# Performance work log

Hardware: AMD Instinct MI355X
Metric: run time of the kernel (lower is better)

## Reference

```python
import jax, jax.numpy as jnp
import numpy as np

D_MODEL = 768
D_INNER = 1536   # expand=2
D_STATE = 16
D_CONV = 4
DT_RANK = 48     # ceil(768/16)
B_SZ, L = 2, 2048


def _mamba(h, in_proj, conv_w, conv_b, xproj, dtproj_w, dtproj_b, A_log, Dskip, out_proj):
    """One Mamba block forward. h: [B, L, d_model]."""
    B = h.shape[0]
    xz = h @ in_proj.T                      # [B, L, 2*d_inner]
    x, z = jnp.split(xz, 2, axis=-1)
    # causal depthwise conv over time
    xc = jnp.transpose(x, (0, 2, 1))        # [B, D, L]
    xc = jax.lax.conv_general_dilated(
        xc, conv_w[:, None, :], (1,), [(D_CONV - 1, 0)],
        dimension_numbers=('NCH', 'OIH', 'NCH'), feature_group_count=D_INNER)
    xc = xc + conv_b[None, :, None]
    x = jax.nn.silu(jnp.transpose(xc, (0, 2, 1)))   # [B, L, D]
    # input-dependent dt, B, C
    dbl = x @ xproj.T                                # [B, L, dt_rank + 2*d_state]
    dt, Bm, Cm = jnp.split(dbl, [DT_RANK, DT_RANK + D_STATE], axis=-1)
    dt = jax.nn.softplus(dt @ dtproj_w.T + dtproj_b) # [B, L, D]
    A = -jnp.exp(A_log)                              # [D, N]

    def step(hst, inp):
        x_t, dt_t, B_t, C_t = inp                    # [B,D],[B,D],[B,N],[B,N]
        dA = jnp.exp(dt_t[..., None] * A)            # [B, D, N]
        hst = hst * dA + dt_t[..., None] * B_t[:, None, :] * x_t[..., None]
        y = jnp.einsum('bdn,bn->bd', hst, C_t)
        return hst, y

    h0 = jnp.zeros((B, D_INNER, D_STATE), dtype=h.dtype)
    xs = (jnp.transpose(x, (1, 0, 2)), jnp.transpose(dt, (1, 0, 2)),
          jnp.transpose(Bm, (1, 0, 2)), jnp.transpose(Cm, (1, 0, 2)))
    _, ys = jax.lax.scan(step, h0, xs)               # ys: [L, B, D]
    y = jnp.transpose(ys, (1, 0, 2)) + x * Dskip
    y = y * jax.nn.silu(z)
    return y @ out_proj.T                            # [B, L, d_model]


def _init_params(key):
    ks = jax.random.split(key, 7)
    s = 0.02
    in_proj = jax.random.normal(ks[0], (2 * D_INNER, D_MODEL)) * s
    conv_w = jax.random.normal(ks[1], (D_INNER, D_CONV)) * 0.2
    conv_b = jnp.zeros((D_INNER,))
    xproj = jax.random.normal(ks[2], (DT_RANK + 2 * D_STATE, D_INNER)) * s
    dtproj_w = jax.random.normal(ks[3], (D_INNER, DT_RANK)) * (DT_RANK ** -0.5)
    dtproj_b = jnp.log(jax.random.uniform(ks[4], (D_INNER,), minval=1e-3, maxval=0.1))
    A_log = jnp.log(jnp.tile(jnp.arange(1, D_STATE + 1, dtype=jnp.float32), (D_INNER, 1)))
    Dskip = jnp.ones((D_INNER,))
    out_proj = jax.random.normal(ks[5], (D_MODEL, D_INNER)) * s
    return in_proj, conv_w, conv_b, xproj, dtproj_w, dtproj_b, A_log, Dskip, out_proj


def setup_inputs() -> dict:
    key = jax.random.key(0)
    k_h, k_f, k_r = jax.random.split(key, 3)
    inp = {'hidden_states': jax.random.normal(k_h, (B_SZ, L, D_MODEL), dtype=jnp.float32)}
    names = ['in_proj', 'conv_w', 'conv_b', 'xproj', 'dtproj_w', 'dtproj_b', 'A_log', 'Dskip', 'out_proj']
    for suf, k in (('_f', k_f), ('_r', k_r)):
        for n, p in zip(names, _init_params(k)):
            inp[n + suf] = p
    return inp


def reference(hidden_states,
              in_proj_f, conv_w_f, conv_b_f, xproj_f, dtproj_w_f, dtproj_b_f, A_log_f, Dskip_f, out_proj_f,
              in_proj_r, conv_w_r, conv_b_r, xproj_r, dtproj_w_r, dtproj_b_r, A_log_r, Dskip_r, out_proj_r):
    out = _mamba(hidden_states, in_proj_f, conv_w_f, conv_b_f, xproj_f,
                 dtproj_w_f, dtproj_b_f, A_log_f, Dskip_f, out_proj_f)
    out_rev = _mamba(hidden_states[:, ::-1, :], in_proj_r, conv_w_r, conv_b_r, xproj_r,
                     dtproj_w_r, dtproj_b_r, A_log_r, Dskip_r, out_proj_r)[:, ::-1, :]
    return out + out_rev
```

## Files before the change

### kernel.cpp

```cpp
#include <hip/hip_runtime.h>
#include <hip/hip_bf16.h>
#include <math.h>

#define L_SEQ 2048
#define B_SZ 2
#define D_MODEL 768
#define D_INNER 1536
#define D_STATE 16
#define DT_RANK 48
#define TC 64
#define NC (L_SEQ / TC)
#define NDG (D_INNER / 256)
#define NSPL 4
#define KCH (D_INNER / NSPL)

typedef short bf16x8 __attribute__((ext_vector_type(8)));
typedef float f32x4 __attribute__((ext_vector_type(4)));

#define GLOAD16(g, l) __builtin_amdgcn_global_load_lds( \
    (const __attribute__((address_space(1))) unsigned*)(g), \
    (__attribute__((address_space(3))) unsigned*)(l), 16, 0, 0)

static __device__ __forceinline__ float siluf(float v) {
  return v / (1.0f + __expf(-v));
}
static __device__ __forceinline__ float softplusf(float v) {
  return fmaxf(v, 0.0f) + log1pf(__expf(-fabsf(v)));
}
static __device__ __forceinline__ unsigned short f2bf_rn(float v) {
  unsigned u = __float_as_uint(v);
  u = (u + 0x7fff + ((u >> 16) & 1)) >> 16;
  return (unsigned short)u;
}

__global__ __launch_bounds__(256) void cvt_all(
    const float* __restrict__ s_h,  unsigned short* __restrict__ hh,  unsigned short* __restrict__ hl,
    const float* __restrict__ s_w0, unsigned short* __restrict__ w0h, unsigned short* __restrict__ w0l,
    const float* __restrict__ s_w1, unsigned short* __restrict__ w1h, unsigned short* __restrict__ w1l,
    const float* __restrict__ s_o0, unsigned short* __restrict__ o0h, unsigned short* __restrict__ o0l,
    const float* __restrict__ s_o1, unsigned short* __restrict__ o1h, unsigned short* __restrict__ o1l)
{
  long j = (long)blockIdx.x * 256 + threadIdx.x;
  const long N0 = 786432, N1 = 589824, N2 = 589824, N3 = 294912;
  const float* src; unsigned short *dh, *dl;
  if (j < N0) { src = s_h; dh = hh; dl = hl; }
  else if ((j -= N0) < N1) { src = s_w0; dh = w0h; dl = w0l; }
  else if ((j -= N1) < N2) { src = s_w1; dh = w1h; dl = w1l; }
  else if ((j -= N2) < N3) { src = s_o0; dh = o0h; dl = o0l; }
  else { j -= N3; src = s_o1; dh = o1h; dl = o1l; }
  float4 v = ((const float4*)src)[j];
  float vv[4] = {v.x, v.y, v.z, v.w};
  unsigned short h4[4], l4[4];
  #pragma unroll
  for (int e = 0; e < 4; ++e) {
    unsigned short hv = f2bf_rn(vv[e]);
    h4[e] = hv;
    l4[e] = f2bf_rn(vv[e] - __uint_as_float((unsigned)hv << 16));
  }
  uint2 ph, pl;
  ph.x = (unsigned)h4[0] | ((unsigned)h4[1] << 16);
  ph.y = (unsigned)h4[2] | ((unsigned)h4[3] << 16);
  pl.x = (unsigned)l4[0] | ((unsigned)l4[1] << 16);
  pl.y = (unsigned)l4[2] | ((unsigned)l4[3] << 16);
  *(uint2*)&dh[j * 4] = ph;
  *(uint2*)&dl[j * 4] = pl;
}

__global__ __launch_bounds__(256) void gemm_inproj(
    const unsigned short* __restrict__ hh, const unsigned short* __restrict__ hl,
    const unsigned short* __restrict__ w0h, const unsigned short* __restrict__ w0l,
    const unsigned short* __restrict__ w1h, const unsigned short* __restrict__ w1l,
    float* __restrict__ xpre, float* __restrict__ zbuf)
{
  __shared__ unsigned short Ah[128 * 32], Al[128 * 32];
  __shared__ unsigned short Wh[128 * 32], Wl[128 * 32];
  const long S1 = (long)B_SZ * L_SEQ * D_INNER;
  const int tid = threadIdx.x;
  const int lane = tid & 63, w = tid >> 6;
  int bid = blockIdx.x;
  int swz = (bid & 7) * 192 + (bid >> 3);
  int dir = swz / 768;
  int rem = swz - dir * 768;
  int mb = rem / 24, nb = rem - (rem / 24) * 24;
  const int m0 = mb * 128, n0 = nb * 128;
  const unsigned short* Whp = dir ? w1h : w0h;
  const unsigned short* Wlp = dir ? w1l : w0l;
  const int ksl = (lane & 3) ^ ((lane >> 3) & 3);
  long aoff[2], woff[2];
  int ldsc[2];
  #pragma unroll
  for (int qq = 0; qq < 2; ++qq) {
    int cq = w * 2 + qq;
    int r = cq * 16 + (lane >> 2);
    int mr = m0 + r;
    int row = dir ? ((mr & ~(L_SEQ - 1)) | ((L_SEQ - 1) - (mr & (L_SEQ - 1)))) : mr;
    aoff[qq] = (long)row * D_MODEL + 8 * ksl;
    woff[qq] = (long)(n0 + r) * D_MODEL + 8 * ksl;
    ldsc[qq] = cq * 512;
  }
  f32x4 acc[4][4];
  #pragma unroll
  for (int i = 0; i < 4; ++i)
    #pragma unroll
    for (int j = 0; j < 4; ++j) acc[i][j] = (f32x4){0.f, 0.f, 0.f, 0.f};
  const int fr = lane & 15, sl = lane >> 4;
  const int wr = w >> 1, wc = w & 1;
  int roffA[4], roffW[4];
  #pragma unroll
  for (int f = 0; f < 4; ++f) {
    int rA = wr * 64 + f * 16 + fr;
    roffA[f] = rA * 32 + ((sl ^ ((rA >> 1) & 3)) * 8);
    int rW = wc * 64 + f * 16 + fr;
    roffW[f] = rW * 32 + ((sl ^ ((rW >> 1) & 3)) * 8);
  }
  for (int k0 = 0; k0 < D_MODEL; k0 += 32) {
    __syncthreads();
    #pragma unroll
    for (int qq = 0; qq < 2; ++qq) {
      GLOAD16(hh + aoff[qq] + k0, &Ah[ldsc[qq]]);
      GLOAD16(hl + aoff[qq] + k0, &Al[ldsc[qq]]);
      GLOAD16(Whp + woff[qq] + k0, &Wh[ldsc[qq]]);
      GLOAD16(Wlp + woff[qq] + k0, &Wl[ldsc[qq]]);
    }
    __syncthreads();
    bf16x8 afh[4], afl[4];
    #pragma unroll
    for (int f = 0; f < 4; ++f) {
      afh[f] = *(const bf16x8*)&Ah[roffA[f]];
      afl[f] = *(const bf16x8*)&Al[roffA[f]];
    }
    #pragma unroll
    for (int fj = 0; fj < 4; ++fj) {
      bf16x8 wfh = *(const bf16x8*)&Wh[roffW[fj]];
      bf16x8 wfl = *(const bf16x8*)&Wl[roffW[fj]];
      #pragma unroll
      for (int fi = 0; fi < 4; ++fi) {
        acc[fi][fj] = __builtin_amdgcn_mfma_f32_16x16x32_bf16(afh[fi], wfh, acc[fi][fj], 0, 0, 0);
        acc[fi][fj] = __builtin_amdgcn_mfma_f32_16x16x32_bf16(afh[fi], wfl, acc[fi][fj], 0, 0, 0);
        acc[fi][fj] = __builtin_amdgcn_mfma_f32_16x16x32_bf16(afl[fi], wfh, acc[fi][fj], 0, 0, 0);
      }
    }
  }
  float* xq = xpre + (long)dir * S1;
  float* zq = zbuf + (long)dir * S1;
  const int fcol = lane & 15, rgrp = lane >> 4;
  #pragma unroll
  for (int fi = 0; fi < 4; ++fi) {
    #pragma unroll
    for (int j = 0; j < 4; ++j) {
      int row = m0 + wr * 64 + fi * 16 + rgrp * 4 + j;
      #pragma unroll
      for (int fj = 0; fj < 4; ++fj) {
        int n = n0 + wc * 64 + fj * 16 + fcol;
        float v = acc[fi][fj][j];
        if (n < D_INNER) xq[(long)row * D_INNER + n] = v;
        else             zq[(long)row * D_INNER + (n - D_INNER)] = v;
      }
    }
  }
}

__global__ __launch_bounds__(256) void gemm_outproj_sk(
    const float* __restrict__ y,
    const unsigned short* __restrict__ wfh, const unsigned short* __restrict__ wfl,
    const unsigned short* __restrict__ wrh, const unsigned short* __restrict__ wrl,
    float* __restrict__ partial)
{
  __shared__ unsigned short Ah[128 * 32], Al[128 * 32];
  __shared__ unsigned short Wh[128 * 32], Wl[128 * 32];
  const long S1 = (long)B_SZ * L_SEQ * D_INNER;
  const int tid = threadIdx.x;
  const int lane = tid & 63, w = tid >> 6;
  int bid = blockIdx.x;
  int swz = (bid & 7) * 96 + (bid >> 3);
  int dir = swz / 384;
  int r1 = swz - dir * 384;
  int ks = r1 / 192;
  int r2 = r1 - ks * 192;
  int mb = r2 / 6, nb = r2 - (r2 / 6) * 6;
  const int m0 = mb * 128, n0 = nb * 128;
  const int kbase = ks * (D_INNER / 2);
  const int srow = tid >> 1, sk = (tid & 1) * 16;
  const int swzA = (srow >> 1) & 3;
  {
  }
  int mr = m0 + srow;
  int rowA = dir ? ((mr & ~(L_SEQ - 1)) | ((L_SEQ - 1) - (mr & (L_SEQ - 1)))) : mr;
  const float* Aptr = y + (long)dir * S1 + (long)rowA * D_INNER + sk;
  const unsigned short* WhP = dir ? wrh : wfh;
  const unsigned short* WlP = dir ? wrl : wfl;
  const int ksl = (lane & 3) ^ ((lane >> 3) & 3);
  long woff[2];
  int ldsc[2];
  #pragma unroll
  for (int qq = 0; qq < 2; ++qq) {
    int cq = w * 2 + qq;
    int r = cq * 16 + (lane >> 2);
    woff[qq] = (long)(n0 + r) * D_INNER + 8 * ksl;
    ldsc[qq] = cq * 512;
  }
  f32x4 acc[4][4];
  #pragma unroll
  for (int i = 0; i < 4; ++i)
    #pragma unroll
    for (int j = 0; j < 4; ++j) acc[i][j] = (f32x4){0.f, 0.f, 0.f, 0.f};
  const int fr = lane & 15, sl = lane >> 4;
  const int wr = w >> 1, wc = w & 1;
  int roffA[4], roffW[4];
  #pragma unroll
  for (int f = 0; f < 4; ++f) {
    int rA = wr * 64 + f * 16 + fr;
    roffA[f] = rA * 32 + ((sl ^ ((rA >> 1) & 3)) * 8);
    int rW = wc * 64 + f * 16 + fr;
    roffW[f] = rW * 32 + ((sl ^ ((rW >> 1) & 3)) * 8);
  }
  for (int k0 = kbase; k0 < kbase + D_INNER / 2; k0 += 32) {
    float4 av[4];
    #pragma unroll
    for (int q = 0; q < 4; ++q) av[q] = *(const float4*)(Aptr + k0 + q * 4);
    unsigned short ah[16], al[16];
    #pragma unroll
    for (int q = 0; q < 4; ++q) {
      float va[4] = {av[q].x, av[q].y, av[q].z, av[q].w};
      #pragma unroll
      for (int e = 0; e < 4; ++e) {
        int i = q * 4 + e;
        unsigned short hv = f2bf_rn(va[e]);
        ah[i] = hv;
        al[i] = f2bf_rn(va[e] - __uint_as_float((unsigned)hv << 16));
      }
    }
    __syncthreads();
    #pragma unroll
    for (int qq = 0; qq < 2; ++qq) {
      GLOAD16(WhP + woff[qq] + k0, &Wh[ldsc[qq]]);
      GLOAD16(WlP + woff[qq] + k0, &Wl[ldsc[qq]]);
    }
    #pragma unroll
    for (int s = 0; s < 2; ++s) {
      int slot = (sk >> 3) + s;
      int off = srow * 32 + ((slot ^ swzA) * 8);
      *(bf16x8*)&Ah[off] = *(const bf16x8*)&ah[s * 8];
      *(bf16x8*)&Al[off] = *(const bf16x8*)&al[s * 8];
    }
    __syncthreads();
    bf16x8 afh[4], afl[4];
    #pragma unroll
    for (int f = 0; f < 4; ++f) {
      afh[f] = *(const bf16x8*)&Ah[roffA[f]];
      afl[f] = *(const bf16x8*)&Al[roffA[f]];
    }
    #pragma unroll
    for (int fj = 0; fj < 4; ++fj) {
      bf16x8 wh = *(const bf16x8*)&Wh[roffW[fj]];
      bf16x8 wl = *(const bf16x8*)&Wl[roffW[fj]];
      #pragma unroll
      for (int fi = 0; fi < 4; ++fi) {
        acc[fi][fj] = __builtin_amdgcn_mfma_f32_16x16x32_bf16(afh[fi], wh, acc[fi][fj], 0, 0, 0);
        acc[fi][fj] = __builtin_amdgcn_mfma_f32_16x16x32_bf16(afh[fi], wl, acc[fi][fj], 0, 0, 0);
        acc[fi][fj] = __builtin_amdgcn_mfma_f32_16x16x32_bf16(afl[fi], wh, acc[fi][fj], 0, 0, 0);
      }
    }
  }
  float* P = partial + (long)(dir * 2 + ks) * (B_SZ * L_SEQ) * D_MODEL;
  const int fcol = lane & 15, rgrp = lane >> 4;
  #pragma unroll
  for (int fi = 0; fi < 4; ++fi) {
    #pragma unroll
    for (int j = 0; j < 4; ++j) {
      int row = m0 + wr * 64 + fi * 16 + rgrp * 4 + j;
      #pragma unroll
      for (int fj = 0; fj < 4; ++fj) {
        int n = n0 + wc * 64 + fj * 16 + fcol;
        P[(long)row * D_MODEL + n] = acc[fi][fj][j];
      }
    }
  }
}

__global__ __launch_bounds__(256) void outproj_reduce(
    const float* __restrict__ partial, float* __restrict__ out)
{
  long i = (long)blockIdx.x * 256 + threadIdx.x;
  const long plane4 = (long)B_SZ * L_SEQ * D_MODEL / 4;
  float4 a = ((const float4*)partial)[i];
  float4 b = ((const float4*)partial)[i + plane4];
  float4 c = ((const float4*)partial)[i + 2 * plane4];
  float4 d = ((const float4*)partial)[i + 3 * plane4];
  float4 s;
  s.x = (a.x + b.x) + (c.x + d.x);
  s.y = (a.y + b.y) + (c.y + d.y);
  s.z = (a.z + b.z) + (c.z + d.z);
  s.w = (a.w + b.w) + (c.w + d.w);
  ((float4*)out)[i] = s;
}

__global__ __launch_bounds__(256) void dtproj(
    const float* __restrict__ dblB,
    const float* __restrict__ w_f, const float* __restrict__ w_r,
    const float* __restrict__ b_f, const float* __restrict__ b_r,
    float* __restrict__ dtOut)
{
  const int dir = blockIdx.z;
  const float* A = dblB + (long)dir * (B_SZ * L_SEQ) * 80;
  const float* W = dir ? w_r : w_f;
  const float* bias = dir ? b_r : b_f;
  float* C0 = dtOut + (long)dir * B_SZ * L_SEQ * D_INNER;
  __shared__ float As[16][132];
  __shared__ float Ws[16][132];
  const int tid = threadIdx.x;
  const int m0 = blockIdx.y * 128, n0 = blockIdx.x * 128;
  const int tx = tid & 15, ty = tid >> 4;
  const int lm = tid >> 1;
  const int lk = (tid & 1) * 8;
  const float* Aptr = A + (long)(m0 + lm) * 80 + lk;
  const float* Wptr = W + (long)(n0 + lm) * DT_RANK + lk;
  float acc[8][8] = {};
  for (int k0 = 0; k0 < DT_RANK; k0 += 16) {
    float4 a0 = *(const float4*)(Aptr + k0);
    float4 a1 = *(const float4*)(Aptr + k0 + 4);
    float4 w0 = *(const float4*)(Wptr + k0);
    float4 w1 = *(const float4*)(Wptr + k0 + 4);
    As[lk + 0][lm] = a0.x; As[lk + 1][lm] = a0.y; As[lk + 2][lm] = a0.z; As[lk + 3][lm] = a0.w;
    As[lk + 4][lm] = a1.x; As[lk + 5][lm] = a1.y; As[lk + 6][lm] = a1.z; As[lk + 7][lm] = a1.w;
    Ws[lk + 0][lm] = w0.x; Ws[lk + 1][lm] = w0.y; Ws[lk + 2][lm] = w0.z; Ws[lk + 3][lm] = w0.w;
    Ws[lk + 4][lm] = w1.x; Ws[lk + 5][lm] = w1.y; Ws[lk + 6][lm] = w1.z; Ws[lk + 7][lm] = w1.w;
    __syncthreads();
    #pragma unroll
    for (int kk = 0; kk < 16; ++kk) {
      float4 av0 = *(const float4*)&As[kk][ty * 4];
      float4 av1 = *(const float4*)&As[kk][64 + ty * 4];
      float4 bv0 = *(const float4*)&Ws[kk][tx * 4];
      float4 bv1 = *(const float4*)&Ws[kk][64 + tx * 4];
      float am[8] = {av0.x, av0.y, av0.z, av0.w, av1.x, av1.y, av1.z, av1.w};
      float bn[8] = {bv0.x, bv0.y, bv0.z, bv0.w, bv1.x, bv1.y, bv1.z, bv1.w};
      #pragma unroll
      for (int i = 0; i < 8; ++i)
        #pragma unroll
        for (int j = 0; j < 8; ++j) acc[i][j] = fmaf(am[i], bn[j], acc[i][j]);
    }
    __syncthreads();
  }
  #pragma unroll
  for (int i = 0; i < 8; ++i) {
    int row = m0 + ty * 4 + (i & 3) + ((i >> 2) << 6);
    #pragma unroll
    for (int j = 0; j < 8; ++j) {
      int n = n0 + tx * 4 + (j & 3) + ((j >> 2) << 6);
      float v = acc[i][j] + bias[n];
      C0[(long)row * D_INNER + n] = softplusf(v);
    }
  }
}

__global__ __launch_bounds__(256) void xproj_splitk(
    const float* __restrict__ X,
    const float* __restrict__ xproj_f, const float* __restrict__ xproj_r,
    float* __restrict__ partial)
{
  const int tid = threadIdx.x;
  const int m0 = blockIdx.x * 64;
  const int kz = blockIdx.y;
  const int dir = blockIdx.z;
  const float* W = dir ? xproj_r : xproj_f;
  const float* A = X + (long)dir * B_SZ * L_SEQ * D_INNER;
  __shared__ float As[16][65];
  __shared__ float Ws[16][81];
  const int lk = tid & 15, lr = tid >> 4;
  const int tx = tid & 15, ty = tid >> 4;
  float acc[4][5] = {};
  const int kbase = kz * KCH;
  for (int k0 = 0; k0 < KCH; k0 += 16) {
    #pragma unroll
    for (int i = 0; i < 4; ++i)
      As[lk][lr + 16 * i] = A[(long)(m0 + lr + 16 * i) * D_INNER + kbase + k0 + lk];
    for (int r = lr; r < 80; r += 16)
      Ws[lk][r] = W[(long)r * D_INNER + kbase + k0 + lk];
    __syncthreads();
    #pragma unroll
    for (int kk = 0; kk < 16; ++kk) {
      float a[4], b[5];
      #pragma unroll
      for (int i = 0; i < 4; ++i) a[i] = As[kk][ty + 16 * i];
      #pragma unroll
      for (int j = 0; j < 5; ++j) b[j] = Ws[kk][tx * 5 + j];
      #pragma unroll
      for (int i = 0; i < 4; ++i)
        #pragma unroll
        for (int j = 0; j < 5; ++j) acc[i][j] = fmaf(a[i], b[j], acc[i][j]);
    }
    __syncthreads();
  }
  float* P = partial + (((long)dir * NSPL + kz) * (B_SZ * L_SEQ) + m0) * 80;
  #pragma unroll
  for (int i = 0; i < 4; ++i)
    #pragma unroll
    for (int j = 0; j < 5; ++j)
      P[(long)(ty + 16 * i) * 80 + tx * 5 + j] = acc[i][j];
}

__global__ __launch_bounds__(256) void xproj_reduce(
    const float* __restrict__ partial, float* __restrict__ dbl)
{
  long idx = (long)blockIdx.x * 256 + threadIdx.x;
  const long plane = (long)B_SZ * L_SEQ * 80;
  long dir = idx / plane;
  long rc = idx % plane;
  const float* P = partial + dir * NSPL * plane + rc;
  float s = 0.f;
  #pragma unroll
  for (int z = 0; z < NSPL; ++z) s += P[z * plane];
  dbl[idx] = s;
}

__global__ __launch_bounds__(256) void conv_silu_v4(
    const float* __restrict__ xpre,
    const float* __restrict__ w_f, const float* __restrict__ b_f,
    const float* __restrict__ w_r, const float* __restrict__ b_r,
    float* __restrict__ xconv)
{
  long i4 = (long)blockIdx.x * 256 + threadIdx.x;
  const long total4 = 2L * B_SZ * L_SEQ * D_INNER / 4;
  if (i4 >= total4) return;
  long idx = i4 * 4;
  int d0 = (int)(idx % D_INNER);
  long r = idx / D_INNER;
  int t = (int)(r & (L_SEQ - 1));
  int dir = (int)(r >> 12);
  const float* w  = dir ? w_r : w_f;
  const float* cb = dir ? b_r : b_f;
  float4 a = *(const float4*)&cb[d0];
  float4 wc[4];
  #pragma unroll
  for (int i = 0; i < 4; ++i) wc[i] = *(const float4*)&w[(d0 + i) * 4];
  #pragma unroll
  for (int k = 0; k < 4; ++k) {
    if (t - 3 + k >= 0) {
      float4 xv = *(const float4*)&xpre[(r - 3 + k) * D_INNER + d0];
      a.x = fmaf(((const float*)&wc[0])[k], xv.x, a.x);
      a.y = fmaf(((const float*)&wc[1])[k], xv.y, a.y);
      a.z = fmaf(((const float*)&wc[2])[k], xv.z, a.z);
      a.w = fmaf(((const float*)&wc[3])[k], xv.w, a.w);
    }
  }
  a.x = siluf(a.x); a.y = siluf(a.y); a.z = siluf(a.z); a.w = siluf(a.w);
  *(float4*)&xconv[idx] = a;
}

__global__ __launch_bounds__(256) void scan_part1(
    const float* __restrict__ dt, const float* __restrict__ x,
    const float* __restrict__ dbl,
    const float* __restrict__ A_log_f, const float* __restrict__ A_log_r,
    float* __restrict__ stateS, float* __restrict__ stateP)
{
  const int tid = threadIdx.x;
  const int chunk = blockIdx.x / NDG;
  const int d = (blockIdx.x % NDG) * 256 + tid;
  const int b = blockIdx.y, dir = blockIdx.z;
  const float* A_log = dir ? A_log_r : A_log_f;
  float Arow[D_STATE];
  #pragma unroll
  for (int n = 0; n < D_STATE; ++n) Arow[n] = -expf(A_log[d * D_STATE + n]);
  float h[D_STATE], P[D_STATE];
  #pragma unroll
  for (int n = 0; n < D_STATE; ++n) { h[n] = 0.f; P[n] = 1.f; }
  const long rowbase = ((long)dir * B_SZ + b) * L_SEQ + (long)chunk * TC;
  __shared__ float bt[TC][D_STATE];
  for (int i = tid; i < TC * D_STATE; i += 256) {
    int t = i >> 4, n = i & 15;
    bt[t][n] = dbl[(rowbase + t) * 80 + 48 + n];
  }
  __syncthreads();
  for (int tj = 0; tj < TC; ++tj) {
    long off = (rowbase + tj) * D_INNER + d;
    float dtv = dt[off];
    float xv = x[off];
    float dtx = dtv * xv;
    #pragma unroll
    for (int n = 0; n < D_STATE; ++n) {
      float dA = __expf(dtv * Arow[n]);
      P[n] *= dA;
      h[n] = fmaf(h[n], dA, dtx * bt[tj][n]);
    }
  }
  long base = ((((long)dir * B_SZ + b) * NC + chunk) * D_INNER + d) * D_STATE;
  #pragma unroll
  for (int n = 0; n < D_STATE; ++n) { stateS[base + n] = h[n]; stateP[base + n] = P[n]; }
}

__global__ __launch_bounds__(256) void scan_fix(
    float* __restrict__ stateS, const float* __restrict__ stateP)
{
  const long idx = (long)blockIdx.x * 256 + threadIdx.x;
  const int DN = D_INNER * D_STATE;
  const long dirb = idx / DN;
  const int dn = (int)(idx % DN);
  long base = dirb * NC * DN + dn;
  float h = 0.f;
  for (int c = 0; c < NC; ++c) {
    long o = base + (long)c * DN;
    float S = stateS[o];
    float Pc = stateP[o];
    stateS[o] = h;
    h = fmaf(h, Pc, S);
  }
}

__global__ __launch_bounds__(256) void scan_part2(
    const float* __restrict__ dt, float* __restrict__ xy,
    const float* __restrict__ dbl, const float* __restrict__ z,
    const float* __restrict__ A_log_f, const float* __restrict__ A_log_r,
    const float* __restrict__ Ds_f, const float* __restrict__ Ds_r,
    const float* __restrict__ stateS)
{
  const int tid = threadIdx.x;
  const int chunk = blockIdx.x / NDG;
  const int d = (blockIdx.x % NDG) * 256 + tid;
  const int b = blockIdx.y, dir = blockIdx.z;
  const float* A_log = dir ? A_log_r : A_log_f;
  const float* Ds = dir ? Ds_r : Ds_f;
  float Arow[D_STATE];
  #pragma unroll
  for (int n = 0; n < D_STATE; ++n) Arow[n] = -expf(A_log[d * D_STATE + n]);
  const float Dd = Ds[d];
  float h[D_STATE];
  long sbase = ((((long)dir * B_SZ + b) * NC + chunk) * D_INNER + d) * D_STATE;
  #pragma unroll
  for (int n = 0; n < D_STATE; ++n) h[n] = stateS[sbase + n];
  const long rowbase = ((long)dir * B_SZ + b) * L_SEQ + (long)chunk * TC;
  __shared__ float bc[TC][2 * D_STATE];
  for (int i = tid; i < TC * 2 * D_STATE; i += 256) {
    int t = i >> 5, n = i & 31;
    bc[t][n] = dbl[(rowbase + t) * 80 + 48 + n];
  }
  __syncthreads();
  for (int tj = 0; tj < TC; ++tj) {
    long off = (rowbase + tj) * D_INNER + d;
    float dtv = dt[off];
    float xv = xy[off];
    float zv = z[off];
    float dtx = dtv * xv;
    float y = 0.f;
    #pragma unroll
    for (int n = 0; n < D_STATE; ++n) {
      float dA = __expf(dtv * Arow[n]);
      h[n] = fmaf(h[n], dA, dtx * bc[tj][n]);
      y = fmaf(h[n], bc[tj][16 + n], y);
    }
    y = fmaf(xv, Dd, y);
    y *= siluf(zv);
    xy[off] = y;
  }
}

extern "C" void kernel_launch(void* const* d_in, const int* in_sizes, int n_in,
                              void* d_out, int out_size, void* d_ws, size_t ws_size,
                              hipStream_t stream) {
  const float* h        = (const float*)d_in[0];
  const float* in_proj[2] = {(const float*)d_in[1], (const float*)d_in[10]};
  const float* conv_w[2]  = {(const float*)d_in[2], (const float*)d_in[11]};
  const float* conv_b[2]  = {(const float*)d_in[3], (const float*)d_in[12]};
  const float* xproj[2]   = {(const float*)d_in[4], (const float*)d_in[13]};
  const float* dtw[2]     = {(const float*)d_in[5], (const float*)d_in[14]};
  const float* dtb[2]     = {(const float*)d_in[6], (const float*)d_in[15]};
  const float* A_log[2]   = {(const float*)d_in[7], (const float*)d_in[16]};
  const float* Dsk[2]     = {(const float*)d_in[8], (const float*)d_in[17]};
  const float* outp[2]    = {(const float*)d_in[9], (const float*)d_in[18]};
  float* out = (float*)d_out;
  float* ws = (float*)d_ws;

  const long S1 = (long)B_SZ * L_SEQ * D_INNER;
  const int M = B_SZ * L_SEQ;
  float* xpre  = ws;
  float* zbuf  = ws + 2 * S1;
  float* xconv = ws + 4 * S1;
  float* dbl   = ws + 6 * S1;
  float* base4 = dbl + 2L * M * 80;

  unsigned short* hh  = (unsigned short*)base4;
  unsigned short* hl  = hh + 3145728;
  unsigned short* w0h = hl + 3145728;
  unsigned short* w0l = w0h + 2359296;
  unsigned short* w1h = w0l + 2359296;
  unsigned short* w1l = w1h + 2359296;
  unsigned short* o0h = w1l + 2359296;
  unsigned short* o0l = o0h + 1179648;
  unsigned short* o1h = o0l + 1179648;
  unsigned short* o1l = o1h + 1179648;
  float* xpartial = base4;
  float* stS = base4;
  float* stP = stS + 3145728;
  float* opartial = xpre;

  dim3 blk(256);

  cvt_all<<<dim3(9984), blk, 0, stream>>>(
      h, hh, hl, in_proj[0], w0h, w0l, in_proj[1], w1h, w1l,
      outp[0], o0h, o0l, outp[1], o1h, o1l);

  gemm_inproj<<<dim3(1536), blk, 0, stream>>>(hh, hl, w0h, w0l, w1h, w1l, xpre, zbuf);

  conv_silu_v4<<<dim3((unsigned)(2 * S1 / 4 / 256)), blk, 0, stream>>>(
      xpre, conv_w[0], conv_b[0], conv_w[1], conv_b[1], xconv);

  {
    dim3 grid(M / 64, NSPL, 2);
    xproj_splitk<<<grid, blk, 0, stream>>>(xconv, xproj[0], xproj[1], xpartial);
    long n = 2L * M * 80;
    xproj_reduce<<<dim3((unsigned)(n / 256)), blk, 0, stream>>>(xpartial, dbl);
  }
  {
    dim3 grid(D_INNER / 128, M / 128, 2);
    dtproj<<<grid, blk, 0, stream>>>(dbl, dtw[0], dtw[1], dtb[0], dtb[1], xpre);
  }
  {
    dim3 grid1(NC * NDG, B_SZ, 2);
    scan_part1<<<grid1, blk, 0, stream>>>(xpre, xconv, dbl,
        A_log[0], A_log[1], stS, stP);
    long nfix = 2L * B_SZ * D_INNER * D_STATE;
    scan_fix<<<dim3((unsigned)(nfix / 256)), blk, 0, stream>>>(stS, stP);
    scan_part2<<<grid1, blk, 0, stream>>>(xpre, xconv, dbl, zbuf,
        A_log[0], A_log[1], Dsk[0], Dsk[1], stS);
  }
  gemm_outproj_sk<<<dim3(768), blk, 0, stream>>>(xconv, o0h, o0l, o1h, o1l, opartial);
  outproj_reduce<<<dim3((unsigned)(M * (long)D_MODEL / 4 / 256)), blk, 0, stream>>>(opartial, out);
}
```

Baseline: 508.7 us.

## Fuse dt projection into scan kernels and emit split-bf16 y for out_proj

Removes the separate dtproj GEMM. Each scan thread now keeps its 48 dt-projection weights in registers and recomputes dt plus softplus per timestep from the dbl row, in both scan passes. The second scan pass writes y already split into bf16 hi/lo halves, so the out-projection GEMM can load A tiles straight into LDS with global_load_lds instead of converting fp32 in the loop. This saves the dt tensor's write and read traffic and one launch, but doubles the dt compute (it runs in both passes) and raises register pressure in the scan kernels.

```diff
diff --git a/kernel.cpp b/kernel.cpp
--- a/kernel.cpp
+++ b/kernel.cpp
@@ -160,10 +160,10 @@
   }
 }
 
-__global__ __launch_bounds__(256) void gemm_outproj_sk(
-    const float* __restrict__ y,
-    const unsigned short* __restrict__ wfh, const unsigned short* __restrict__ wfl,
-    const unsigned short* __restrict__ wrh, const unsigned short* __restrict__ wrl,
+__global__ __launch_bounds__(256) void gemm_outproj_pl(
+    const unsigned short* __restrict__ yh, const unsigned short* __restrict__ yl,
+    const unsigned short* __restrict__ o0h, const unsigned short* __restrict__ o0l,
+    const unsigned short* __restrict__ o1h, const unsigned short* __restrict__ o1l,
     float* __restrict__ partial)
 {
   __shared__ unsigned short Ah[128 * 32], Al[128 * 32];
@@ -180,23 +180,21 @@
   int mb = r2 / 6, nb = r2 - (r2 / 6) * 6;
   const int m0 = mb * 128, n0 = nb * 128;
   const int kbase = ks * (D_INNER / 2);
-  const int srow = tid >> 1, sk = (tid & 1) * 16;
-  const int swzA = (srow >> 1) & 3;
-  {
-  }
-  int mr = m0 + srow;
-  int rowA = dir ? ((mr & ~(L_SEQ - 1)) | ((L_SEQ - 1) - (mr & (L_SEQ - 1)))) : mr;
-  const float* Aptr = y + (long)dir * S1 + (long)rowA * D_INNER + sk;
-  const unsigned short* WhP = dir ? wrh : wfh;
-  const unsigned short* WlP = dir ? wrl : wfl;
+  const unsigned short* Ahp = yh + (long)dir * S1;
+  const unsigned short* Alp = yl + (long)dir * S1;
+  const unsigned short* Whp = dir ? o1h : o0h;
+  const unsigned short* Wlp = dir ? o1l : o0l;
   const int ksl = (lane & 3) ^ ((lane >> 3) & 3);
-  long woff[2];
+  long aoff[2], woff[2];
   int ldsc[2];
   #pragma unroll
   for (int qq = 0; qq < 2; ++qq) {
     int cq = w * 2 + qq;
     int r = cq * 16 + (lane >> 2);
-    woff[qq] = (long)(n0 + r) * D_INNER + 8 * ksl;
+    int mr = m0 + r;
+    int row = dir ? ((mr & ~(L_SEQ - 1)) | ((L_SEQ - 1) - (mr & (L_SEQ - 1)))) : mr;
+    aoff[qq] = (long)row * D_INNER + 8 * ksl + kbase;
+    woff[qq] = (long)(n0 + r) * D_INNER + 8 * ksl + kbase;
     ldsc[qq] = cq * 512;
   }
   f32x4 acc[4][4];
@@ -214,34 +212,14 @@
     int rW = wc * 64 + f * 16 + fr;
     roffW[f] = rW * 32 + ((sl ^ ((rW >> 1) & 3)) * 8);
   }
-  for (int k0 = kbase; k0 < kbase + D_INNER / 2; k0 += 32) {
-    float4 av[4];
-    #pragma unroll
-    for (int q = 0; q < 4; ++q) av[q] = *(const float4*)(Aptr + k0 + q * 4);
-    unsigned short ah[16], al[16];
-    #pragma unroll
-    for (int q = 0; q < 4; ++q) {
-      float va[4] = {av[q].x, av[q].y, av[q].z, av[q].w};
-      #pragma unroll
-      for (int e = 0; e < 4; ++e) {
-        int i = q * 4 + e;
-        unsigned short hv = f2bf_rn(va[e]);
-        ah[i] = hv;
-        al[i] = f2bf_rn(va[e] - __uint_as_float((unsigned)hv << 16));
-      }
-    }
+  for (int k0 = 0; k0 < D_INNER / 2; k0 += 32) {
     __syncthreads();
     #pragma unroll
     for (int qq = 0; qq < 2; ++qq) {
-      GLOAD16(WhP + woff[qq] + k0, &Wh[ldsc[qq]]);
-      GLOAD16(WlP + woff[qq] + k0, &Wl[ldsc[qq]]);
-    }
-    #pragma unroll
-    for (int s = 0; s < 2; ++s) {
-      int slot = (sk >> 3) + s;
-      int off = srow * 32 + ((slot ^ swzA) * 8);
-      *(bf16x8*)&Ah[off] = *(const bf16x8*)&ah[s * 8];
-      *(bf16x8*)&Al[off] = *(const bf16x8*)&al[s * 8];
+      GLOAD16(Ahp + aoff[qq] + k0, &Ah[ldsc[qq]]);
+      GLOAD16(Alp + aoff[qq] + k0, &Al[ldsc[qq]]);
+      GLOAD16(Whp + woff[qq] + k0, &Wh[ldsc[qq]]);
+      GLOAD16(Wlp + woff[qq] + k0, &Wl[ldsc[qq]]);
     }
     __syncthreads();
     bf16x8 afh[4], afl[4];
@@ -252,13 +230,13 @@
     }
     #pragma unroll
     for (int fj = 0; fj < 4; ++fj) {
-      bf16x8 wh = *(const bf16x8*)&Wh[roffW[fj]];
-      bf16x8 wl = *(const bf16x8*)&Wl[roffW[fj]];
+      bf16x8 wfh = *(const bf16x8*)&Wh[roffW[fj]];
+      bf16x8 wfl = *(const bf16x8*)&Wl[roffW[fj]];
       #pragma unroll
       for (int fi = 0; fi < 4; ++fi) {
-        acc[fi][fj] = __builtin_amdgcn_mfma_f32_16x16x32_bf16(afh[fi], wh, acc[fi][fj], 0, 0, 0);
-        acc[fi][fj] = __builtin_amdgcn_mfma_f32_16x16x32_bf16(afh[fi], wl, acc[fi][fj], 0, 0, 0);
-        acc[fi][fj] = __builtin_amdgcn_mfma_f32_16x16x32_bf16(afl[fi], wh, acc[fi][fj], 0, 0, 0);
+        acc[fi][fj] = __builtin_amdgcn_mfma_f32_16x16x32_bf16(afh[fi], wfh, acc[fi][fj], 0, 0, 0);
+        acc[fi][fj] = __builtin_amdgcn_mfma_f32_16x16x32_bf16(afh[fi], wfl, acc[fi][fj], 0, 0, 0);
+        acc[fi][fj] = __builtin_amdgcn_mfma_f32_16x16x32_bf16(afl[fi], wfh, acc[fi][fj], 0, 0, 0);
       }
     }
   }
@@ -293,64 +271,6 @@
   s.z = (a.z + b.z) + (c.z + d.z);
   s.w = (a.w + b.w) + (c.w + d.w);
   ((float4*)out)[i] = s;
-}
-
-__global__ __launch_bounds__(256) void dtproj(
-    const float* __restrict__ dblB,
-    const float* __restrict__ w_f, const float* __restrict__ w_r,
-    const float* __restrict__ b_f, const float* __restrict__ b_r,
-    float* __restrict__ dtOut)
-{
-  const int dir = blockIdx.z;
-  const float* A = dblB + (long)dir * (B_SZ * L_SEQ) * 80;
-  const float* W = dir ? w_r : w_f;
-  const float* bias = dir ? b_r : b_f;
-  float* C0 = dtOut + (long)dir * B_SZ * L_SEQ * D_INNER;
-  __shared__ float As[16][132];
-  __shared__ float Ws[16][132];
-  const int tid = threadIdx.x;
-  const int m0 = blockIdx.y * 128, n0 = blockIdx.x * 128;
-  const int tx = tid & 15, ty = tid >> 4;
-  const int lm = tid >> 1;
-  const int lk = (tid & 1) * 8;
-  const float* Aptr = A + (long)(m0 + lm) * 80 + lk;
-  const float* Wptr = W + (long)(n0 + lm) * DT_RANK + lk;
-  float acc[8][8] = {};
-  for (int k0 = 0; k0 < DT_RANK; k0 += 16) {
-    float4 a0 = *(const float4*)(Aptr + k0);
-    float4 a1 = *(const float4*)(Aptr + k0 + 4);
-    float4 w0 = *(const float4*)(Wptr + k0);
-    float4 w1 = *(const float4*)(Wptr + k0 + 4);
-    As[lk + 0][lm] = a0.x; As[lk + 1][lm] = a0.y; As[lk + 2][lm] = a0.z; As[lk + 3][lm] = a0.w;
-    As[lk + 4][lm] = a1.x; As[lk + 5][lm] = a1.y; As[lk + 6][lm] = a1.z; As[lk + 7][lm] = a1.w;
-    Ws[lk + 0][lm] = w0.x; Ws[lk + 1][lm] = w0.y; Ws[lk + 2][lm] = w0.z; Ws[lk + 3][lm] = w0.w;
-    Ws[lk + 4][lm] = w1.x; Ws[lk + 5][lm] = w1.y; Ws[lk + 6][lm] = w1.z; Ws[lk + 7][lm] = w1.w;
-    __syncthreads();
-    #pragma unroll
-    for (int kk = 0; kk < 16; ++kk) {
-      float4 av0 = *(const float4*)&As[kk][ty * 4];
-      float4 av1 = *(const float4*)&As[kk][64 + ty * 4];
-      float4 bv0 = *(const float4*)&Ws[kk][tx * 4];
-      float4 bv1 = *(const float4*)&Ws[kk][64 + tx * 4];
-      float am[8] = {av0.x, av0.y, av0.z, av0.w, av1.x, av1.y, av1.z, av1.w};
-      float bn[8] = {bv0.x, bv0.y, bv0.z, bv0.w, bv1.x, bv1.y, bv1.z, bv1.w};
-      #pragma unroll
-      for (int i = 0; i < 8; ++i)
-        #pragma unroll
-        for (int j = 0; j < 8; ++j) acc[i][j] = fmaf(am[i], bn[j], acc[i][j]);
-    }
-    __syncthreads();
-  }
-  #pragma unroll
-  for (int i = 0; i < 8; ++i) {
-    int row = m0 + ty * 4 + (i & 3) + ((i >> 2) << 6);
-    #pragma unroll
-    for (int j = 0; j < 8; ++j) {
-      int n = n0 + tx * 4 + (j & 3) + ((j >> 2) << 6);
-      float v = acc[i][j] + bias[n];
-      C0[(long)row * D_INNER + n] = softplusf(v);
-    }
-  }
 }
 
 __global__ __launch_bounds__(256) void xproj_splitk(
@@ -426,9 +346,8 @@
   int d0 = (int)(idx % D_INNER);
   long r = idx / D_INNER;
   int t = (int)(r & (L_SEQ - 1));
-  int dir = (int)(r >> 12);
-  const float* w  = dir ? w_r : w_f;
-  const float* cb = dir ? b_r : b_f;
+  const float* w  = (r >> 12) ? w_r : w_f;
+  const float* cb = (r >> 12) ? b_r : b_f;
   float4 a = *(const float4*)&cb[d0];
   float4 wc[4];
   #pragma unroll
@@ -447,9 +366,10 @@
   *(float4*)&xconv[idx] = a;
 }
 
-__global__ __launch_bounds__(256) void scan_part1(
-    const float* __restrict__ dt, const float* __restrict__ x,
-    const float* __restrict__ dbl,
+__global__ __launch_bounds__(256) void scan_mega1(
+    const float* __restrict__ x, const float* __restrict__ dbl,
+    const float* __restrict__ dtw_f, const float* __restrict__ dtw_r,
+    const float* __restrict__ dtb_f, const float* __restrict__ dtb_r,
     const float* __restrict__ A_log_f, const float* __restrict__ A_log_r,
     float* __restrict__ stateS, float* __restrict__ stateP)
 {
@@ -458,6 +378,12 @@
   const int d = (blockIdx.x % NDG) * 256 + tid;
   const int b = blockIdx.y, dir = blockIdx.z;
   const float* A_log = dir ? A_log_r : A_log_f;
+  const float* dtw   = dir ? dtw_r : dtw_f;
+  const float dtbv   = (dir ? dtb_r : dtb_f)[d];
+  float wreg[48];
+  #pragma unroll
+  for (int q = 0; q < 12; ++q)
+    *(float4*)&wreg[q * 4] = *(const float4*)&dtw[d * DT_RANK + q * 4];
   float Arow[D_STATE];
   #pragma unroll
   for (int n = 0; n < D_STATE; ++n) Arow[n] = -expf(A_log[d * D_STATE + n]);
@@ -465,22 +391,29 @@
   #pragma unroll
   for (int n = 0; n < D_STATE; ++n) { h[n] = 0.f; P[n] = 1.f; }
   const long rowbase = ((long)dir * B_SZ + b) * L_SEQ + (long)chunk * TC;
-  __shared__ float bt[TC][D_STATE];
-  for (int i = tid; i < TC * D_STATE; i += 256) {
-    int t = i >> 4, n = i & 15;
-    bt[t][n] = dbl[(rowbase + t) * 80 + 48 + n];
-  }
-  __syncthreads();
   for (int tj = 0; tj < TC; ++tj) {
-    long off = (rowbase + tj) * D_INNER + d;
-    float dtv = dt[off];
-    float xv = x[off];
+    const float* br = dbl + (rowbase + tj) * 80;
+    float dtacc = 0.f;
+    #pragma unroll
+    for (int q = 0; q < 12; ++q) {
+      float4 v = *(const float4*)(br + q * 4);
+      dtacc = fmaf(v.x, wreg[q * 4 + 0], dtacc);
+      dtacc = fmaf(v.y, wreg[q * 4 + 1], dtacc);
+      dtacc = fmaf(v.z, wreg[q * 4 + 2], dtacc);
+      dtacc = fmaf(v.w, wreg[q * 4 + 3], dtacc);
+    }
+    float dtv = softplusf(dtacc + dtbv);
+    float xv = x[(rowbase + tj) * D_INNER + d];
     float dtx = dtv * xv;
+    float bc[D_STATE];
+    #pragma unroll
+    for (int q = 0; q < 4; ++q)
+      *(float4*)&bc[q * 4] = *(const float4*)(br + 48 + q * 4);
     #pragma unroll
     for (int n = 0; n < D_STATE; ++n) {
       float dA = __expf(dtv * Arow[n]);
       P[n] *= dA;
-      h[n] = fmaf(h[n], dA, dtx * bt[tj][n]);
+      h[n] = fmaf(h[n], dA, dtx * bc[n]);
     }
   }
   long base = ((((long)dir * B_SZ + b) * NC + chunk) * D_INNER + d) * D_STATE;
@@ -506,50 +439,68 @@
   }
 }
 
-__global__ __launch_bounds__(256) void scan_part2(
-    const float* __restrict__ dt, float* __restrict__ xy,
-    const float* __restrict__ dbl, const float* __restrict__ z,
+__global__ __launch_bounds__(256) void scan_mega2(
+    const float* __restrict__ x, const float* __restrict__ dbl,
+    const float* __restrict__ z,
+    const float* __restrict__ dtw_f, const float* __restrict__ dtw_r,
+    const float* __restrict__ dtb_f, const float* __restrict__ dtb_r,
     const float* __restrict__ A_log_f, const float* __restrict__ A_log_r,
     const float* __restrict__ Ds_f, const float* __restrict__ Ds_r,
-    const float* __restrict__ stateS)
+    const float* __restrict__ stateS,
+    unsigned short* __restrict__ yh, unsigned short* __restrict__ yl)
 {
   const int tid = threadIdx.x;
   const int chunk = blockIdx.x / NDG;
   const int d = (blockIdx.x % NDG) * 256 + tid;
   const int b = blockIdx.y, dir = blockIdx.z;
   const float* A_log = dir ? A_log_r : A_log_f;
-  const float* Ds = dir ? Ds_r : Ds_f;
+  const float* dtw   = dir ? dtw_r : dtw_f;
+  const float dtbv   = (dir ? dtb_r : dtb_f)[d];
+  const float Dd     = (dir ? Ds_r : Ds_f)[d];
+  float wreg[48];
+  #pragma unroll
+  for (int q = 0; q < 12; ++q)
+    *(float4*)&wreg[q * 4] = *(const float4*)&dtw[d * DT_RANK + q * 4];
   float Arow[D_STATE];
   #pragma unroll
   for (int n = 0; n < D_STATE; ++n) Arow[n] = -expf(A_log[d * D_STATE + n]);
-  const float Dd = Ds[d];
   float h[D_STATE];
   long sbase = ((((long)dir * B_SZ + b) * NC + chunk) * D_INNER + d) * D_STATE;
   #pragma unroll
   for (int n = 0; n < D_STATE; ++n) h[n] = stateS[sbase + n];
   const long rowbase = ((long)dir * B_SZ + b) * L_SEQ + (long)chunk * TC;
-  __shared__ float bc[TC][2 * D_STATE];
-  for (int i = tid; i < TC * 2 * D_STATE; i += 256) {
-    int t = i >> 5, n = i & 31;
-    bc[t][n] = dbl[(rowbase + t) * 80 + 48 + n];
-  }
-  __syncthreads();
   for (int tj = 0; tj < TC; ++tj) {
+    const float* br = dbl + (rowbase + tj) * 80;
+    float dtacc = 0.f;
+    #pragma unroll
+    for (int q = 0; q < 12; ++q) {
+      float4 v = *(const float4*)(br + q * 4);
+      dtacc = fmaf(v.x, wreg[q * 4 + 0], dtacc);
+      dtacc = fmaf(v.y, wreg[q * 4 + 1], dtacc);
+      dtacc = fmaf(v.z, wreg[q * 4 + 2], dtacc);
+      dtacc = fmaf(v.w, wreg[q * 4 + 3], dtacc);
+    }
+    float dtv = softplusf(dtacc + dtbv);
     long off = (rowbase + tj) * D_INNER + d;
-    float dtv = dt[off];
-    float xv = xy[off];
+    float xv = x[off];
     float zv = z[off];
     float dtx = dtv * xv;
+    float bc[2 * D_STATE];
+    #pragma unroll
+    for (int q = 0; q < 8; ++q)
+      *(float4*)&bc[q * 4] = *(const float4*)(br + 48 + q * 4);
     float y = 0.f;
     #pragma unroll
     for (int n = 0; n < D_STATE; ++n) {
       float dA = __expf(dtv * Arow[n]);
-      h[n] = fmaf(h[n], dA, dtx * bc[tj][n]);
-      y = fmaf(h[n], bc[tj][16 + n], y);
+      h[n] = fmaf(h[n], dA, dtx * bc[n]);
+      y = fmaf(h[n], bc[16 + n], y);
     }
     y = fmaf(xv, Dd, y);
     y *= siluf(zv);
-    xy[off] = y;
+    unsigned short hv = f2bf_rn(y);
+    yh[off] = hv;
+    yl[off] = f2bf_rn(y - __uint_as_float((unsigned)hv << 16));
   }
 }
 
@@ -590,7 +541,9 @@
   float* xpartial = base4;
   float* stS = base4;
   float* stP = stS + 3145728;
-  float* opartial = xpre;
+  unsigned short* yh = (unsigned short*)xpre;
+  unsigned short* yl = yh + 2 * S1;
+  float* opartial = xconv;
 
   dim3 blk(256);
 
@@ -610,18 +563,15 @@
     xproj_reduce<<<dim3((unsigned)(n / 256)), blk, 0, stream>>>(xpartial, dbl);
   }
   {
-    dim3 grid(D_INNER / 128, M / 128, 2);
-    dtproj<<<grid, blk, 0, stream>>>(dbl, dtw[0], dtw[1], dtb[0], dtb[1], xpre);
-  }
-  {
     dim3 grid1(NC * NDG, B_SZ, 2);
-    scan_part1<<<grid1, blk, 0, stream>>>(xpre, xconv, dbl,
-        A_log[0], A_log[1], stS, stP);
+    scan_mega1<<<grid1, blk, 0, stream>>>(xconv, dbl,
+        dtw[0], dtw[1], dtb[0], dtb[1], A_log[0], A_log[1], stS, stP);
     long nfix = 2L * B_SZ * D_INNER * D_STATE;
     scan_fix<<<dim3((unsigned)(nfix / 256)), blk, 0, stream>>>(stS, stP);
-    scan_part2<<<grid1, blk, 0, stream>>>(xpre, xconv, dbl, zbuf,
-        A_log[0], A_log[1], Dsk[0], Dsk[1], stS);
-  }
-  gemm_outproj_sk<<<dim3(768), blk, 0, stream>>>(xconv, o0h, o0l, o1h, o1l, opartial);
+    scan_mega2<<<grid1, blk, 0, stream>>>(xconv, dbl, zbuf,
+        dtw[0], dtw[1], dtb[0], dtb[1], A_log[0], A_log[1],
+        Dsk[0], Dsk[1], stS, yh, yl);
+  }
+  gemm_outproj_pl<<<dim3(768), blk, 0, stream>>>(yh, yl, o0h, o0l, o1h, o1l, opartial);
   outproj_reduce<<<dim3((unsigned)(M * (long)D_MODEL / 4 / 256)), blk, 0, stream>>>(opartial, out);
 }
```

Result: slower. 527.3 us (+3.7%).
